# Kernel optimization log

Measured on AMD Instinct MI355X. Metric: run time of the kernel, lower is better.

## Reference

```python
import jax, jax.numpy as jnp
from jax import lax
import numpy as np

EPS_COS = 1e-8   # cosine-similarity eps (matches F.cosine_similarity default scale)
EPS_IN = 1e-5    # InstanceNorm2d default eps
NEG = -1e9


def _conv3(x, w, b):
    # x: [B,C,H,W], w: [O,I,3,3]
    y = lax.conv_general_dilated(x, w, (1, 1), 'SAME',
                                 dimension_numbers=('NCHW', 'OIHW', 'NCHW'))
    return y + b[None, :, None, None]


def _inorm(x):
    m = jnp.mean(x, axis=(2, 3), keepdims=True)
    v = jnp.var(x, axis=(2, 3), keepdims=True)
    return (x - m) * lax.rsqrt(v + EPS_IN)


def _shift(former, latter, mask):
    # former/latter: [B,C,H,W]; mask: [H,W] int (1 = hole).
    # For every masked pixel, find the most cosine-similar UNMASKED pixel in the
    # latter (known-region encoder) features and copy the former feature from it.
    B, C, H, W = former.shape
    L = H * W
    lat = lax.stop_gradient(latter).reshape(B, C, L)           # attention is non-differentiable
    latn = lat / (jnp.linalg.norm(lat, axis=1, keepdims=True) + EPS_COS)
    sim = jnp.einsum('bcm,bcn->bmn', latn, latn)               # [B,L,L] query m -> key n
    mflat = mask.reshape(L) > 0
    sim = jnp.where(mflat[None, None, :], NEG, sim)            # keys must be unmasked
    idx = jnp.argmax(sim, axis=-1)                             # [B,L]
    fflat = former.reshape(B, C, L)
    gathered = jnp.take_along_axis(fflat, jnp.broadcast_to(idx[:, None, :], (B, C, L)), axis=2)
    shift = jnp.where(mflat[None, None, :], gathered, 0.0)     # zeros outside the hole
    return shift.reshape(B, C, H, W)


def setup_inputs() -> dict:
    key = jax.random.key(0)
    ks = jax.random.split(key, 6)
    B, C, H, W = 8, 256, 64, 64
    inp = jax.random.normal(ks[0], (B, 2 * C, H, W), dtype=jnp.float32)
    mask = jax.random.randint(ks[1], (H, W), 0, 2, dtype=jnp.int32)
    s1 = 1.0 / float(np.sqrt(2 * C * 9))
    s2 = 1.0 / float(np.sqrt(C * 9))
    W1 = jax.random.uniform(ks[2], (C, 2 * C, 3, 3), jnp.float32, -s1, s1)
    b1 = jax.random.uniform(ks[3], (C,), jnp.float32, -s1, s1)
    W2 = jax.random.uniform(ks[4], (C, C, 3, 3), jnp.float32, -s2, s2)
    b2 = jax.random.uniform(ks[5], (C,), jnp.float32, -s2, s2)
    return {"input": inp, "mask": mask, "W1": W1, "b1": b1, "W2": W2, "b2": b2}


def reference(input, mask, W1, b1, W2, b2):
    C = input.shape[1] // 2
    F_c = input[:, :C]          # former (decoder) features
    F_s = input[:, C:]          # latter (encoder) features
    F_shift = _shift(F_c, F_s, mask)
    F_fuse = F_c * F_shift
    F_com = jnp.concatenate([F_c, F_fuse], axis=1)             # [B,2C,H,W]
    h = jax.nn.relu(_inorm(_conv3(F_com, W1, b1)))
    res = _inorm(_conv3(h, W2, b2))
    return jnp.concatenate([F_c + res, F_s], axis=1)
```

## Files before the change

### kernel.cpp

```cpp
#include <hip/hip_runtime.h>
#include <hip/hip_bf16.h>
#include <math.h>

#define L 4096
#define C 256
#define B 8

typedef __attribute__((ext_vector_type(8))) short bf16x8;
typedef __attribute__((ext_vector_type(8))) ushort u16x8;
typedef __attribute__((ext_vector_type(4))) float f32x4;

__device__ inline ushort f2bu(float f) { __hip_bfloat16 h = __float2bfloat16(f); return *(ushort*)&h; }
__device__ inline float bu2f(ushort u) { __hip_bfloat16 h; *(ushort*)&h = u; return __bfloat162float(h); }

__global__ __launch_bounds__(256) void compact_mask(
    const int* __restrict__ mask, int* __restrict__ counts,
    int* __restrict__ maskedOrig, int* __restrict__ unmaskOrig,
    int* __restrict__ posOf)
{
    __shared__ int smM[256], smU[256];
    int t = threadIdx.x;
    int flags[16];
    int cm = 0, cu = 0;
    for (int k = 0; k < 16; ++k) {
        int l = t * 16 + k;
        int f = mask[l] > 0;
        flags[k] = f;
        cm += f; cu += !f;
    }
    smM[t] = cm; smU[t] = cu;
    __syncthreads();
    for (int off = 1; off < 256; off <<= 1) {
        int vM = 0, vU = 0;
        if (t >= off) { vM = smM[t - off]; vU = smU[t - off]; }
        __syncthreads();
        smM[t] += vM; smU[t] += vU;
        __syncthreads();
    }
    if (t == 255) { counts[0] = smM[255]; counts[1] = smU[255]; }
    int pm = smM[t] - cm, pu = smU[t] - cu;
    for (int k = 0; k < 16; ++k) {
        int l = t * 16 + k;
        if (flags[k]) { maskedOrig[pm] = l; posOf[l] = pm; pm++; }
        else          { unmaskOrig[pu] = l; posOf[l] = pu; pu++; }
    }
}

__global__ __launch_bounds__(256) void norm_transpose(
    const float* __restrict__ input, const int* __restrict__ mask,
    const int* __restrict__ counts, const int* __restrict__ posOf,
    ushort* __restrict__ fsnh, ushort* __restrict__ fsnl)
{
    int bx = blockIdx.x;
    int b = bx >> 7;
    int l0 = (bx & 127) * 32;
    __shared__ float tile[256 * 33];
    __shared__ float part[8 * 33];
    __shared__ float denom[32];
    __shared__ int   rowdst[32];
    int t = threadIdx.x;
    int lsub = t & 31, cg = t >> 5;
    for (int cc = 0; cc < 256; cc += 8) {
        int c = cc + cg;
        tile[c * 33 + lsub] = input[((size_t)(b * 512 + 256 + c)) * L + l0 + lsub];
    }
    __syncthreads();
    float s = 0.f;
    for (int c = cg; c < 256; c += 8) { float v = tile[c * 33 + lsub]; s = fmaf(v, v, s); }
    part[cg * 33 + lsub] = s;
    __syncthreads();
    if (t < 32) {
        float s2 = 0.f;
        for (int g = 0; g < 8; ++g) s2 += part[g * 33 + t];
        denom[t] = sqrtf(s2) + 1e-8f;
        int l = l0 + t;
        int Nm = counts[0];
        rowdst[t] = (mask[l] > 0) ? posOf[l] : (Nm + posOf[l]);
    }
    __syncthreads();
    for (int ls = 0; ls < 32; ++ls) {
        int r = rowdst[ls];
        float d = denom[ls];
        float val = tile[t * 33 + ls] / d;
        ushort h = f2bu(val);
        float hf = bu2f(h);
        ushort lo = f2bu(val - hf);
        size_t o = ((size_t)b * L + r) * C + t;
        fsnh[o] = h;
        fsnl[o] = lo;
    }
}

__global__ __launch_bounds__(256, 2) void sim_argmax_v2(
    const ushort* __restrict__ hi, const ushort* __restrict__ lo,
    const int* __restrict__ counts,
    float* __restrict__ pval, int* __restrict__ pidx)
{
    __shared__ ushort ldsB[2 * 64 * 256];
    const int Nm = counts[0], Nu = counts[1];
    const int b = blockIdx.z;
    const int m0 = blockIdx.y * 64;
    const int half = blockIdx.x;
    const int t = threadIdx.x;
    const int w = t >> 6, l = t & 63;
    const int lm = l & 15, lk = l >> 4;
    const int key = (lm & 7) << 4;

    const int nct = (Nu + 63) >> 6;
    const int hs = (nct + 1) >> 1;
    const int cA = half * hs;
    const int cB = (half ? nct : hs);

    float bestv[4]; int bestn[4];
#pragma unroll
    for (int r = 0; r < 4; ++r) { bestv[r] = -3e38f; bestn[r] = 0; }

    if (m0 < Nm && cA < cB) {
        const char* bytesH = (const char*)hi;
        const char* bytesL = (const char*)lo;
        const size_t bL = (size_t)b * L;
        char* ldsc = (char*)ldsB;

#define STAGE(cc) do { \
    size_t gb = (bL + (size_t)Nm + (size_t)(cc) * 64) * 512; \
    _Pragma("unroll") \
    for (int i = 0; i < 8; ++i) { \
        int j = w * 8 + i; \
        int x = j * 1024 + l * 16; \
        int sx = x ^ (((x >> 9) & 7) << 4); \
        __builtin_amdgcn_global_load_lds((const __attribute__((address_space(1))) unsigned*)(bytesH + gb + sx), \
            (__attribute__((address_space(3))) unsigned*)(ldsc + j * 1024), 16, 0, 0); \
        __builtin_amdgcn_global_load_lds((const __attribute__((address_space(1))) unsigned*)(bytesL + gb + sx), \
            (__attribute__((address_space(3))) unsigned*)(ldsc + 32768 + j * 1024), 16, 0, 0); \
    } \
} while (0)

        STAGE(cA);

        const int rA = m0 + w * 16 + lm;
        bf16x8 ah[8], al[8];
        {
            const ushort* aH = hi + (bL + rA) * C + lk * 8;
            const ushort* aL = lo + (bL + rA) * C + lk * 8;
#pragma unroll
            for (int ks = 0; ks < 8; ++ks) {
                ah[ks] = *(const bf16x8*)(aH + ks * 32);
                al[ks] = *(const bf16x8*)(aL + ks * 32);
            }
        }

        for (int c = cA; c < cB; ++c) {
            asm volatile("s_waitcnt vmcnt(0)" ::: "memory");
            __syncthreads();
            f32x4 acc[4];
#pragma unroll
            for (int nf = 0; nf < 4; ++nf) acc[nf] = (f32x4){0.f, 0.f, 0.f, 0.f};
#pragma unroll
            for (int ks = 0; ks < 8; ++ks) {
                bf16x8 bh[4], bl[4];
#pragma unroll
                for (int nf = 0; nf < 4; ++nf) {
                    int row = nf * 16 + lm;
                    int addr = row * 512 + ((ks * 64 + lk * 16) ^ key);
                    bh[nf] = *(const bf16x8*)(ldsc + addr);
                    bl[nf] = *(const bf16x8*)(ldsc + 32768 + addr);
                }
#pragma unroll
                for (int nf = 0; nf < 4; ++nf)
                    acc[nf] = __builtin_amdgcn_mfma_f32_16x16x32_bf16(ah[ks], bh[nf], acc[nf], 0, 0, 0);
#pragma unroll
                for (int nf = 0; nf < 4; ++nf)
                    acc[nf] = __builtin_amdgcn_mfma_f32_16x16x32_bf16(ah[ks], bl[nf], acc[nf], 0, 0, 0);
#pragma unroll
                for (int nf = 0; nf < 4; ++nf)
                    acc[nf] = __builtin_amdgcn_mfma_f32_16x16x32_bf16(al[ks], bh[nf], acc[nf], 0, 0, 0);
            }
            __syncthreads();
            if (c + 1 < cB) STAGE(c + 1);
            int nbase = c * 64;
#pragma unroll
            for (int r = 0; r < 4; ++r) {
#pragma unroll
                for (int nf = 0; nf < 4; ++nf) {
                    int n = nbase + nf * 16 + lm;
                    float v = acc[nf][r];
                    if (n < Nu && v > bestv[r]) { bestv[r] = v; bestn[r] = n; }
                }
            }
        }
#undef STAGE
    }

    if (m0 >= Nm) return;
#pragma unroll
    for (int r = 0; r < 4; ++r) {
        float bv = bestv[r]; int bn = bestn[r];
#pragma unroll
        for (int mk = 1; mk < 16; mk <<= 1) {
            float ov = __shfl_xor(bv, mk, 64);
            int   on = __shfl_xor(bn, mk, 64);
            if (ov > bv || (ov == bv && on < bn)) { bv = ov; bn = on; }
        }
        if (lm == 0) {
            int m = m0 + w * 16 + lk * 4 + r;
            size_t o = ((size_t)(b * 4096 + m)) * 2 + half;
            pval[o] = bv; pidx[o] = bn;
        }
    }
}

__global__ __launch_bounds__(256) void argmax_reduce2(
    const float* __restrict__ pval, const int* __restrict__ pidx,
    const int* __restrict__ counts, const int* __restrict__ maskedOrig,
    const int* __restrict__ unmaskOrig, int* __restrict__ idxmap)
{
    int i = blockIdx.x * 256 + threadIdx.x;
    int b = i >> 12, m = i & 4095;
    int Nm = counts[0];
    if (m >= Nm) return;
    size_t base = (size_t)i * 2;
    float bv = pval[base]; int bn = pidx[base];
    float v1 = pval[base + 1];
    if (v1 > bv) { bv = v1; bn = pidx[base + 1]; }
    idxmap[(b << 12) + maskedOrig[m]] = unmaskOrig[bn];
}

__global__ __launch_bounds__(256) void wprep(
    const float* __restrict__ W1, const float* __restrict__ W2,
    ushort* __restrict__ W1bf, ushort* __restrict__ W2bf)
{
    int gid = blockIdx.x * 256 + threadIdx.x;
    const int N1 = 256 * 512 * 9;
    const int N2 = 256 * 256 * 9;
    if (gid < N1) {
        int ci = gid & 511; int rest = gid >> 9;
        int tau = rest % 9; int co = rest / 9;
        W1bf[gid] = f2bu(W1[((size_t)(co * 512 + ci)) * 9 + tau]);
    } else if (gid < N1 + N2) {
        int g = gid - N1;
        int ci = g & 255; int rest = g >> 8;
        int tau = rest % 9; int co = rest / 9;
        W2bf[g] = f2bu(W2[((size_t)(co * 256 + ci)) * 9 + tau]);
    }
}

__global__ __launch_bounds__(256) void in_prep1(
    const float* __restrict__ input, ushort* __restrict__ inT)
{
    int b = blockIdx.y;
    int p0 = blockIdx.x * 32;
    __shared__ float tile[256][33];
    int t = threadIdx.x;
    int pq = t & 7;
    for (int cc = 0; cc < 256; cc += 32) {
        int ci = cc + (t >> 3);
        float4 v = *(const float4*)(input + ((size_t)(b * 512 + ci)) * L + p0 + pq * 4);
        tile[ci][pq * 4 + 0] = v.x; tile[ci][pq * 4 + 1] = v.y;
        tile[ci][pq * 4 + 2] = v.z; tile[ci][pq * 4 + 3] = v.w;
    }
    __syncthreads();
    int c8 = t & 31;
    for (int pp = 0; pp < 32; pp += 8) {
        int pixloc = pp + (t >> 5);
        u16x8 u;
#pragma unroll
        for (int j = 0; j < 8; ++j) u[j] = f2bu(tile[c8 * 8 + j][pixloc]);
        *(u16x8*)(inT + ((size_t)(b * 4096 + p0 + pixloc)) * 512 + c8 * 8) = u;
    }
}

__global__ __launch_bounds__(256) void in_prep2(
    ushort* __restrict__ inT, const int* __restrict__ mask,
    const int* __restrict__ idxmap)
{
    int gid = blockIdx.x * 256 + threadIdx.x;
    int c8 = gid & 31;
    int pix = (gid >> 5) & 4095;
    int b = gid >> 17;
    u16x8 out8;
    if (mask[pix] > 0) {
        int n = idxmap[(b << 12) + pix];
        const ushort* rp = inT + ((size_t)(b * 4096 + pix)) * 512 + c8 * 8;
        const ushort* rn = inT + ((size_t)(b * 4096 + n)) * 512 + c8 * 8;
        u16x8 a = *(const u16x8*)rp;
        u16x8 bb = *(const u16x8*)rn;
#pragma unroll
        for (int j = 0; j < 8; ++j) out8[j] = f2bu(bu2f(a[j]) * bu2f(bb[j]));
    } else {
#pragma unroll
        for (int j = 0; j < 8; ++j) out8[j] = 0;
    }
    *(u16x8*)(inT + ((size_t)(b * 4096 + pix)) * 512 + 256 + c8 * 8) = out8;
}

template<int CKROW>
__global__ __launch_bounds__(256, 2) void conv_mfma(
    const ushort* __restrict__ Abf, const ushort* __restrict__ Wbf,
    float* __restrict__ outF, ushort* __restrict__ outH,
    float* __restrict__ psum, int store32)
{
    __shared__ float4 ldsv[62208 / 16];
    char* lds = (char*)ldsv;
    char* ldsB = lds + 25344;
    const int t = threadIdx.x;
    const int w = t >> 6;
    const int l = t & 63;
    const int lm = l & 15, lk = l >> 4;
    const int b = blockIdx.z;
    const int y0 = blockIdx.x * 4;
    const int c0 = blockIdx.y * 64;
    const int yw = y0 + w;
    const size_t abase = (size_t)b * 4096 * CKROW;

    f32x4 acc[4][4];
#pragma unroll
    for (int g = 0; g < 4; ++g)
#pragma unroll
        for (int nf = 0; nf < 4; ++nf) acc[g][nf] = (f32x4){0.f, 0.f, 0.f, 0.f};

    if (t < 48) {
        int r = t >> 3;
        int cX = ((t >> 2) & 1) ? 65 : 0;
        int k8 = t & 3;
        *(float4*)(lds + (r * 66 + cX) * 64 + ((k8 * 16) ^ ((cX & 3) << 4))) = (float4){0.f,0.f,0.f,0.f};
    }

    const int NKC = CKROW / 32;
    for (int kc = 0; kc < NKC; ++kc) {
        __syncthreads();
        {
            int x = t >> 2;
            int k8 = t & 3;
            int cX = x + 1;
            char* dbase = lds + cX * 64 + ((k8 * 16) ^ ((cX & 3) << 4));
#pragma unroll
            for (int r = 0; r < 6; ++r) {
                int yy = y0 - 1 + r;
                float4 v;
                if (yy >= 0 && yy < 64)
                    v = *(const float4*)(Abf + abase + (size_t)(yy * 64 + x) * CKROW + kc * 32 + k8 * 8);
                else
                    v = (float4){0.f, 0.f, 0.f, 0.f};
                *(float4*)(dbase + r * (66 * 64)) = v;
            }
        }
        {
            int cl = t >> 2;
            int k8 = t & 3;
            char* dbase = ldsB + cl * 64 + ((k8 * 16) ^ ((cl & 3) << 4));
            const ushort* sbase = Wbf + ((size_t)(c0 + cl) * 9) * CKROW + kc * 32 + k8 * 8;
#pragma unroll
            for (int tau = 0; tau < 9; ++tau) {
                *(float4*)(dbase + tau * (64 * 64)) = *(const float4*)(sbase + (size_t)tau * CKROW);
            }
        }
        __syncthreads();
#pragma unroll
        for (int ky = 0; ky < 3; ++ky) {
            int r = w + ky;
#pragma unroll
            for (int kx = 0; kx < 3; ++kx) {
                int tau = ky * 3 + kx;
                bf16x8 bfr[4];
#pragma unroll
                for (int nf = 0; nf < 4; ++nf) {
                    int cl = nf * 16 + lm;
                    bfr[nf] = *(bf16x8*)(ldsB + (tau * 64 + cl) * 64 + ((lk * 16) ^ ((cl & 3) << 4)));
                }
#pragma unroll
                for (int g = 0; g < 4; ++g) {
                    int cX = g * 16 + lm + kx;
                    bf16x8 afr = *(bf16x8*)(lds + (r * 66 + cX) * 64 + ((lk * 16) ^ ((cX & 3) << 4)));
#pragma unroll
                    for (int nf = 0; nf < 4; ++nf)
                        acc[g][nf] = __builtin_amdgcn_mfma_f32_16x16x32_bf16(afr, bfr[nf], acc[g][nf], 0, 0, 0);
                }
            }
        }
    }

    if (store32) {
#pragma unroll
        for (int g = 0; g < 4; ++g)
#pragma unroll
            for (int nf = 0; nf < 4; ++nf) {
                int cout = c0 + nf * 16 + lm;
#pragma unroll
                for (int r = 0; r < 4; ++r) {
                    int pix = yw * 64 + g * 16 + lk * 4 + r;
                    outF[((size_t)(b * 4096 + pix)) * 256 + cout] = acc[g][nf][r];
                }
            }
    } else {
#pragma unroll
        for (int g = 0; g < 4; ++g)
#pragma unroll
            for (int nf = 0; nf < 4; ++nf) {
                int cout = c0 + nf * 16 + lm;
#pragma unroll
                for (int r = 0; r < 4; ++r) {
                    int pix = yw * 64 + g * 16 + lk * 4 + r;
                    outH[((size_t)(b * 4096 + pix)) * 256 + cout] = f2bu(acc[g][nf][r]);
                }
            }
    }

    float s[4], q[4];
#pragma unroll
    for (int nf = 0; nf < 4; ++nf) {
        float ss = 0.f, qq = 0.f;
#pragma unroll
        for (int g = 0; g < 4; ++g)
#pragma unroll
            for (int r = 0; r < 4; ++r) { float v = acc[g][nf][r]; ss += v; qq = fmaf(v, v, qq); }
        ss += __shfl_xor(ss, 16, 64); ss += __shfl_xor(ss, 32, 64);
        qq += __shfl_xor(qq, 16, 64); qq += __shfl_xor(qq, 32, 64);
        s[nf] = ss; q[nf] = qq;
    }
    __syncthreads();
    float* S = (float*)lds;
    float* Q = (float*)(lds + 1024);
    if (l < 16) {
#pragma unroll
        for (int nf = 0; nf < 4; ++nf) {
            S[w * 64 + nf * 16 + l] = s[nf];
            Q[w * 64 + nf * 16 + l] = q[nf];
        }
    }
    __syncthreads();
    if (t < 64) {
        float ts = 0.f, tq = 0.f;
#pragma unroll
        for (int w2 = 0; w2 < 4; ++w2) { ts += S[w2 * 64 + t]; tq += Q[w2 * 64 + t]; }
        size_t o = (((size_t)(b * 256 + c0 + t)) * 16 + blockIdx.x) * 2;
        psum[o] = ts; psum[o + 1] = tq;
    }
}

__global__ __launch_bounds__(256) void stats_reduce(
    const float* __restrict__ psum, float* __restrict__ mrs)
{
    int b = blockIdx.x;
    int c = threadIdx.x;
    float s = 0.f, q = 0.f;
    size_t base = ((size_t)(b * 256 + c)) * 16;
    for (int k = 0; k < 16; ++k) { s += psum[(base + k) * 2]; q += psum[(base + k) * 2 + 1]; }
    float mean = s * (1.f / 4096.f);
    float var = q * (1.f / 4096.f) - mean * mean;
    float rs = rsqrtf(var + 1e-5f);
    mrs[(b * 256 + c) * 2] = mean;
    mrs[(b * 256 + c) * 2 + 1] = rs;
}

__global__ __launch_bounds__(256) void norm1_apply(
    const float* __restrict__ h_raw, const float* __restrict__ mrs,
    ushort* __restrict__ hbf)
{
    int gid = blockIdx.x * 256 + threadIdx.x;
    int c4 = gid & 63;
    int pix = (gid >> 6) & 4095;
    int b = gid >> 18;
    float4 hv = *(const float4*)(h_raw + (((size_t)(b * 4096 + pix)) << 8) + c4 * 4);
    const float4* mv = (const float4*)(mrs + (size_t)b * 512);
    float4 m0 = mv[c4 * 2];
    float4 m1 = mv[c4 * 2 + 1];
    float z0 = (hv.x - m0.x) * m0.y;
    float z1 = (hv.y - m0.z) * m0.w;
    float z2 = (hv.z - m1.x) * m1.y;
    float z3 = (hv.w - m1.z) * m1.w;
    ushort4 o;
    o.x = f2bu(z0 > 0.f ? z0 : 0.f);
    o.y = f2bu(z1 > 0.f ? z1 : 0.f);
    o.z = f2bu(z2 > 0.f ? z2 : 0.f);
    o.w = f2bu(z3 > 0.f ? z3 : 0.f);
    *(ushort4*)(hbf + (((size_t)(b * 4096 + pix)) << 8) + c4 * 4) = o;
}

__global__ __launch_bounds__(256) void finalize(
    const ushort* __restrict__ resbf, const float* __restrict__ mrs,
    const float* __restrict__ input, float* __restrict__ out)
{
    int b = blockIdx.y;
    int p0 = blockIdx.x * 32;
    __shared__ float tileT[256][33];
    int t = threadIdx.x;
    int c8 = t & 31;
    for (int pp = 0; pp < 32; pp += 8) {
        int pixloc = pp + (t >> 5);
        u16x8 u = *(const u16x8*)(resbf + (((size_t)(b * 4096 + p0 + pixloc)) << 8) + c8 * 8);
#pragma unroll
        for (int j = 0; j < 8; ++j) tileT[c8 * 8 + j][pixloc] = bu2f(u[j]);
    }
    __syncthreads();
    int pq = t & 7;
    for (int cc = 0; cc < 256; cc += 32) {
        int c = cc + (t >> 3);
        float m = mrs[(b * 256 + c) * 2];
        float rs = mrs[(b * 256 + c) * 2 + 1];
        size_t off = ((size_t)(b * 512 + c)) * L + p0 + pq * 4;
        float4 f = *(const float4*)(input + off);
        float4 o;
        o.x = f.x + (tileT[c][pq * 4 + 0] - m) * rs;
        o.y = f.y + (tileT[c][pq * 4 + 1] - m) * rs;
        o.z = f.z + (tileT[c][pq * 4 + 2] - m) * rs;
        o.w = f.w + (tileT[c][pq * 4 + 3] - m) * rs;
        *(float4*)(out + off) = o;
    }
}

__global__ __launch_bounds__(256) void copy_fs(
    const float* __restrict__ input, float* __restrict__ out)
{
    size_t i = (size_t)blockIdx.x * 256 + threadIdx.x;
    size_t b = i >> 18;
    size_t r = i & 262143;
    size_t o = ((size_t)(b * 512 + 256)) * 1024 + r;
    const float4* s = (const float4*)input;
    float4* d = (float4*)out;
    d[o] = s[o];
}

extern "C" void kernel_launch(void* const* d_in, const int* in_sizes, int n_in,
                              void* d_out, int out_size, void* d_ws, size_t ws_size,
                              hipStream_t stream) {
    const float* input = (const float*)d_in[0];
    const int*   mask  = (const int*)d_in[1];
    const float* W1    = (const float*)d_in[2];
    const float* W2    = (const float*)d_in[4];
    float* out = (float*)d_out;
    (void)in_sizes; (void)n_in; (void)out_size; (void)ws_size;

    char* ob = (char*)d_out;
    char* wp = (char*)d_ws;

    ushort* fsnh = (ushort*)ob;
    ushort* fsnl = (ushort*)(ob + 16777216);
    float*  pval = (float*)(ob + 33554432);
    int*    pidx = (int*)(ob + 37748736);
    ushort* inT  = (ushort*)ob;
    float*  h_raw = (float*)(ob + 33554432);
    ushort* hbf  = (ushort*)ob;

    ushort* resbf  = (ushort*)wp;
    ushort* W1bf   = (ushort*)(wp + 16777216);
    ushort* W2bf   = (ushort*)(wp + 19136512);
    float*  psum1  = (float*)(wp + 20316160);
    float*  psum2  = (float*)(wp + 20578304);
    float*  mrs1   = (float*)(wp + 20840448);
    float*  mrs2   = (float*)(wp + 20856832);
    int* counts     = (int*)(wp + 20873216);
    int* maskedOrig = counts + 4;
    int* unmaskOrig = maskedOrig + L;
    int* posOf      = unmaskOrig + L;
    int* idxmap     = posOf + L;

    compact_mask<<<1, 256, 0, stream>>>(mask, counts, maskedOrig, unmaskOrig, posOf);
    norm_transpose<<<1024, 256, 0, stream>>>(input, mask, counts, posOf, fsnh, fsnl);
    sim_argmax_v2<<<dim3(2, 64, 8), 256, 0, stream>>>(fsnh, fsnl, counts, pval, pidx);
    argmax_reduce2<<<128, 256, 0, stream>>>(pval, pidx, counts, maskedOrig, unmaskOrig, idxmap);
    wprep<<<6912, 256, 0, stream>>>(W1, W2, W1bf, W2bf);
    in_prep1<<<dim3(128, 8), 256, 0, stream>>>(input, inT);
    in_prep2<<<4096, 256, 0, stream>>>(inT, mask, idxmap);
    conv_mfma<512><<<dim3(16, 4, 8), 256, 0, stream>>>(inT, W1bf, h_raw, (ushort*)nullptr, psum1, 1);
    stats_reduce<<<8, 256, 0, stream>>>(psum1, mrs1);
    norm1_apply<<<8192, 256, 0, stream>>>(h_raw, mrs1, hbf);
    conv_mfma<256><<<dim3(16, 4, 8), 256, 0, stream>>>(hbf, W2bf, (float*)nullptr, resbf, psum2, 0);
    stats_reduce<<<8, 256, 0, stream>>>(psum2, mrs2);
    finalize<<<dim3(128, 8), 256, 0, stream>>>(resbf, mrs2, input, out);
    copy_fs<<<8192, 256, 0, stream>>>(input, out);
}
```

Baseline: 282.1 us.

## Double-buffer sim-argmax LDS tiles with 512-thread blocks; store conv1 output as bf16

```diff
diff --git a/kernel.cpp b/kernel.cpp
--- a/kernel.cpp
+++ b/kernel.cpp
@@ -91,12 +91,12 @@
     }
 }
 
-__global__ __launch_bounds__(256, 2) void sim_argmax_v2(
+__global__ __launch_bounds__(512, 1) void sim_argmax_v3(
     const ushort* __restrict__ hi, const ushort* __restrict__ lo,
     const int* __restrict__ counts,
     float* __restrict__ pval, int* __restrict__ pidx)
 {
-    __shared__ ushort ldsB[2 * 64 * 256];
+    __shared__ ushort ldsB[65536];
     const int Nm = counts[0], Nu = counts[1];
     const int b = blockIdx.z;
     const int m0 = blockIdx.y * 64;
@@ -104,97 +104,99 @@
     const int t = threadIdx.x;
     const int w = t >> 6, l = t & 63;
     const int lm = l & 15, lk = l >> 4;
-    const int key = (lm & 7) << 4;
+    const int mh = w & 1, nq = w >> 1;
 
     const int nct = (Nu + 63) >> 6;
     const int hs = (nct + 1) >> 1;
-    const int cA = half * hs;
-    const int cB = (half ? nct : hs);
-
-    float bestv[4]; int bestn[4];
-#pragma unroll
-    for (int r = 0; r < 4; ++r) { bestv[r] = -3e38f; bestn[r] = 0; }
-
-    if (m0 < Nm && cA < cB) {
+    const int cA = half * hs, cB = half ? nct : hs;
+
+    float bestv0[4], bestv1[4]; int bestn0[4], bestn1[4];
+#pragma unroll
+    for (int r = 0; r < 4; ++r) {
+        bestv0[r] = -3e38f; bestn0[r] = 0;
+        bestv1[r] = -3e38f; bestn1[r] = 0;
+    }
+
+    if (m0 >= Nm) return;
+
+    if (cA < cB) {
+        char* ldsc = (char*)ldsB;
         const char* bytesH = (const char*)hi;
         const char* bytesL = (const char*)lo;
         const size_t bL = (size_t)b * L;
-        char* ldsc = (char*)ldsB;
-
-#define STAGE(cc) do { \
+
+#define STAGE(bufofs, cc) do { \
     size_t gb = (bL + (size_t)Nm + (size_t)(cc) * 64) * 512; \
     _Pragma("unroll") \
-    for (int i = 0; i < 8; ++i) { \
-        int j = w * 8 + i; \
-        int x = j * 1024 + l * 16; \
-        int sx = x ^ (((x >> 9) & 7) << 4); \
+    for (int i = 0; i < 4; ++i) { \
+        int xu = w * 4096 + i * 1024; \
+        int xl = xu + l * 16; \
+        int sx = xl ^ (((xl >> 9) & 7) << 4); \
         __builtin_amdgcn_global_load_lds((const __attribute__((address_space(1))) unsigned*)(bytesH + gb + sx), \
-            (__attribute__((address_space(3))) unsigned*)(ldsc + j * 1024), 16, 0, 0); \
+            (__attribute__((address_space(3))) unsigned*)(ldsc + (bufofs) + xu), 16, 0, 0); \
         __builtin_amdgcn_global_load_lds((const __attribute__((address_space(1))) unsigned*)(bytesL + gb + sx), \
-            (__attribute__((address_space(3))) unsigned*)(ldsc + 32768 + j * 1024), 16, 0, 0); \
+            (__attribute__((address_space(3))) unsigned*)(ldsc + (bufofs) + 32768 + xu), 16, 0, 0); \
     } \
 } while (0)
 
-        STAGE(cA);
-
-        const int rA = m0 + w * 16 + lm;
-        bf16x8 ah[8], al[8];
+        STAGE(0, cA);
+
+        const int rA0 = m0 + mh * 32 + lm;
+        bf16x8 ah0[8], al0[8], ah1[8], al1[8];
         {
-            const ushort* aH = hi + (bL + rA) * C + lk * 8;
-            const ushort* aL = lo + (bL + rA) * C + lk * 8;
+            const ushort* aH0 = hi + (bL + rA0) * C + lk * 8;
+            const ushort* aL0 = lo + (bL + rA0) * C + lk * 8;
+            const ushort* aH1 = aH0 + 16 * C;
+            const ushort* aL1 = aL0 + 16 * C;
 #pragma unroll
             for (int ks = 0; ks < 8; ++ks) {
-                ah[ks] = *(const bf16x8*)(aH + ks * 32);
-                al[ks] = *(const bf16x8*)(aL + ks * 32);
-            }
-        }
+                ah0[ks] = *(const bf16x8*)(aH0 + ks * 32);
+                al0[ks] = *(const bf16x8*)(aL0 + ks * 32);
+                ah1[ks] = *(const bf16x8*)(aH1 + ks * 32);
+                al1[ks] = *(const bf16x8*)(aL1 + ks * 32);
+            }
+        }
+
+        const int row = nq * 16 + lm;
+        const int key = (row & 7) << 4;
 
         for (int c = cA; c < cB; ++c) {
+            int bo = ((c - cA) & 1) * 65536;
             asm volatile("s_waitcnt vmcnt(0)" ::: "memory");
             __syncthreads();
-            f32x4 acc[4];
-#pragma unroll
-            for (int nf = 0; nf < 4; ++nf) acc[nf] = (f32x4){0.f, 0.f, 0.f, 0.f};
+            if (c + 1 < cB) STAGE(bo ^ 65536, c + 1);
+            const char* bhp = ldsc + bo + row * 512;
+            const char* blp = bhp + 32768;
+            f32x4 acc0 = (f32x4){0.f, 0.f, 0.f, 0.f};
+            f32x4 acc1 = (f32x4){0.f, 0.f, 0.f, 0.f};
 #pragma unroll
             for (int ks = 0; ks < 8; ++ks) {
-                bf16x8 bh[4], bl[4];
-#pragma unroll
-                for (int nf = 0; nf < 4; ++nf) {
-                    int row = nf * 16 + lm;
-                    int addr = row * 512 + ((ks * 64 + lk * 16) ^ key);
-                    bh[nf] = *(const bf16x8*)(ldsc + addr);
-                    bl[nf] = *(const bf16x8*)(ldsc + 32768 + addr);
-                }
-#pragma unroll
-                for (int nf = 0; nf < 4; ++nf)
-                    acc[nf] = __builtin_amdgcn_mfma_f32_16x16x32_bf16(ah[ks], bh[nf], acc[nf], 0, 0, 0);
-#pragma unroll
-                for (int nf = 0; nf < 4; ++nf)
-                    acc[nf] = __builtin_amdgcn_mfma_f32_16x16x32_bf16(ah[ks], bl[nf], acc[nf], 0, 0, 0);
-#pragma unroll
-                for (int nf = 0; nf < 4; ++nf)
-                    acc[nf] = __builtin_amdgcn_mfma_f32_16x16x32_bf16(al[ks], bh[nf], acc[nf], 0, 0, 0);
-            }
-            __syncthreads();
-            if (c + 1 < cB) STAGE(c + 1);
-            int nbase = c * 64;
+                int off = (ks * 64 + lk * 16) ^ key;
+                bf16x8 bh = *(const bf16x8*)(bhp + off);
+                bf16x8 bl = *(const bf16x8*)(blp + off);
+                acc0 = __builtin_amdgcn_mfma_f32_16x16x32_bf16(ah0[ks], bh, acc0, 0, 0, 0);
+                acc0 = __builtin_amdgcn_mfma_f32_16x16x32_bf16(ah0[ks], bl, acc0, 0, 0, 0);
+                acc0 = __builtin_amdgcn_mfma_f32_16x16x32_bf16(al0[ks], bh, acc0, 0, 0, 0);
+                acc1 = __builtin_amdgcn_mfma_f32_16x16x32_bf16(ah1[ks], bh, acc1, 0, 0, 0);
+                acc1 = __builtin_amdgcn_mfma_f32_16x16x32_bf16(ah1[ks], bl, acc1, 0, 0, 0);
+                acc1 = __builtin_amdgcn_mfma_f32_16x16x32_bf16(al1[ks], bh, acc1, 0, 0, 0);
+            }
+            int n = c * 64 + nq * 16 + lm;
+            bool nv = n < Nu;
 #pragma unroll
             for (int r = 0; r < 4; ++r) {
-#pragma unroll
-                for (int nf = 0; nf < 4; ++nf) {
-                    int n = nbase + nf * 16 + lm;
-                    float v = acc[nf][r];
-                    if (n < Nu && v > bestv[r]) { bestv[r] = v; bestn[r] = n; }
-                }
+                float v0 = acc0[r];
+                if (nv && v0 > bestv0[r]) { bestv0[r] = v0; bestn0[r] = n; }
+                float v1 = acc1[r];
+                if (nv && v1 > bestv1[r]) { bestv1[r] = v1; bestn1[r] = n; }
             }
         }
 #undef STAGE
     }
 
-    if (m0 >= Nm) return;
 #pragma unroll
     for (int r = 0; r < 4; ++r) {
-        float bv = bestv[r]; int bn = bestn[r];
+        float bv = bestv0[r]; int bn = bestn0[r];
 #pragma unroll
         for (int mk = 1; mk < 16; mk <<= 1) {
             float ov = __shfl_xor(bv, mk, 64);
@@ -202,26 +204,40 @@
             if (ov > bv || (ov == bv && on < bn)) { bv = ov; bn = on; }
         }
         if (lm == 0) {
-            int m = m0 + w * 16 + lk * 4 + r;
-            size_t o = ((size_t)(b * 4096 + m)) * 2 + half;
+            int m = m0 + mh * 32 + lk * 4 + r;
+            size_t o = ((size_t)(b * 4096 + m)) * 8 + half * 4 + nq;
             pval[o] = bv; pidx[o] = bn;
         }
-    }
-}
-
-__global__ __launch_bounds__(256) void argmax_reduce2(
+        bv = bestv1[r]; bn = bestn1[r];
+#pragma unroll
+        for (int mk = 1; mk < 16; mk <<= 1) {
+            float ov = __shfl_xor(bv, mk, 64);
+            int   on = __shfl_xor(bn, mk, 64);
+            if (ov > bv || (ov == bv && on < bn)) { bv = ov; bn = on; }
+        }
+        if (lm == 0) {
+            int m = m0 + mh * 32 + 16 + lk * 4 + r;
+            size_t o = ((size_t)(b * 4096 + m)) * 8 + half * 4 + nq;
+            pval[o] = bv; pidx[o] = bn;
+        }
+    }
+}
+
+__global__ __launch_bounds__(256) void argmax_reduce8(
     const float* __restrict__ pval, const int* __restrict__ pidx,
     const int* __restrict__ counts, const int* __restrict__ maskedOrig,
     const int* __restrict__ unmaskOrig, int* __restrict__ idxmap)
 {
     int i = blockIdx.x * 256 + threadIdx.x;
     int b = i >> 12, m = i & 4095;
-    int Nm = counts[0];
-    if (m >= Nm) return;
-    size_t base = (size_t)i * 2;
+    if (m >= counts[0]) return;
+    size_t base = (size_t)i * 8;
     float bv = pval[base]; int bn = pidx[base];
-    float v1 = pval[base + 1];
-    if (v1 > bv) { bv = v1; bn = pidx[base + 1]; }
+#pragma unroll
+    for (int p = 1; p < 8; ++p) {
+        float v = pval[base + p]; int n2 = pidx[base + p];
+        if (v > bv || (v == bv && n2 < bn)) { bv = v; bn = n2; }
+    }
     idxmap[(b << 12) + maskedOrig[m]] = unmaskOrig[bn];
 }
 
@@ -453,27 +469,23 @@
 }
 
 __global__ __launch_bounds__(256) void norm1_apply(
-    const float* __restrict__ h_raw, const float* __restrict__ mrs,
+    const ushort* __restrict__ hraw, const float* __restrict__ mrs,
     ushort* __restrict__ hbf)
 {
     int gid = blockIdx.x * 256 + threadIdx.x;
-    int c4 = gid & 63;
-    int pix = (gid >> 6) & 4095;
-    int b = gid >> 18;
-    float4 hv = *(const float4*)(h_raw + (((size_t)(b * 4096 + pix)) << 8) + c4 * 4);
-    const float4* mv = (const float4*)(mrs + (size_t)b * 512);
-    float4 m0 = mv[c4 * 2];
-    float4 m1 = mv[c4 * 2 + 1];
-    float z0 = (hv.x - m0.x) * m0.y;
-    float z1 = (hv.y - m0.z) * m0.w;
-    float z2 = (hv.z - m1.x) * m1.y;
-    float z3 = (hv.w - m1.z) * m1.w;
-    ushort4 o;
-    o.x = f2bu(z0 > 0.f ? z0 : 0.f);
-    o.y = f2bu(z1 > 0.f ? z1 : 0.f);
-    o.z = f2bu(z2 > 0.f ? z2 : 0.f);
-    o.w = f2bu(z3 > 0.f ? z3 : 0.f);
-    *(ushort4*)(hbf + (((size_t)(b * 4096 + pix)) << 8) + c4 * 4) = o;
+    int c8 = gid & 31;
+    int pix = (gid >> 5) & 4095;
+    int b = gid >> 17;
+    size_t off = (((size_t)(b * 4096 + pix)) << 8) + c8 * 8;
+    u16x8 v = *(const u16x8*)(hraw + off);
+    const float* mb = mrs + (size_t)b * 512 + c8 * 16;
+    u16x8 o;
+#pragma unroll
+    for (int j = 0; j < 8; ++j) {
+        float z = (bu2f(v[j]) - mb[j * 2]) * mb[j * 2 + 1];
+        o[j] = f2bu(z > 0.f ? z : 0.f);
+    }
+    *(u16x8*)(hbf + off) = o;
 }
 
 __global__ __launch_bounds__(256) void finalize(
@@ -538,7 +550,7 @@
     float*  pval = (float*)(ob + 33554432);
     int*    pidx = (int*)(ob + 37748736);
     ushort* inT  = (ushort*)ob;
-    float*  h_raw = (float*)(ob + 33554432);
+    ushort* hraw = (ushort*)(ob + 33554432);
     ushort* hbf  = (ushort*)ob;
 
     ushort* resbf  = (ushort*)wp;
@@ -556,14 +568,14 @@
 
     compact_mask<<<1, 256, 0, stream>>>(mask, counts, maskedOrig, unmaskOrig, posOf);
     norm_transpose<<<1024, 256, 0, stream>>>(input, mask, counts, posOf, fsnh, fsnl);
-    sim_argmax_v2<<<dim3(2, 64, 8), 256, 0, stream>>>(fsnh, fsnl, counts, pval, pidx);
-    argmax_reduce2<<<128, 256, 0, stream>>>(pval, pidx, counts, maskedOrig, unmaskOrig, idxmap);
+    sim_argmax_v3<<<dim3(2, 64, 8), 512, 0, stream>>>(fsnh, fsnl, counts, pval, pidx);
+    argmax_reduce8<<<128, 256, 0, stream>>>(pval, pidx, counts, maskedOrig, unmaskOrig, idxmap);
     wprep<<<6912, 256, 0, stream>>>(W1, W2, W1bf, W2bf);
     in_prep1<<<dim3(128, 8), 256, 0, stream>>>(input, inT);
     in_prep2<<<4096, 256, 0, stream>>>(inT, mask, idxmap);
-    conv_mfma<512><<<dim3(16, 4, 8), 256, 0, stream>>>(inT, W1bf, h_raw, (ushort*)nullptr, psum1, 1);
+    conv_mfma<512><<<dim3(16, 4, 8), 256, 0, stream>>>(inT, W1bf, (float*)nullptr, hraw, psum1, 0);
     stats_reduce<<<8, 256, 0, stream>>>(psum1, mrs1);
-    norm1_apply<<<8192, 256, 0, stream>>>(h_raw, mrs1, hbf);
+    norm1_apply<<<4096, 256, 0, stream>>>(hraw, mrs1, hbf);
     conv_mfma<256><<<dim3(16, 4, 8), 256, 0, stream>>>(hbf, W2bf, (float*)nullptr, resbf, psum2, 0);
     stats_reduce<<<8, 256, 0, stream>>>(psum2, mrs2);
     finalize<<<dim3(128, 8), 256, 0, stream>>>(resbf, mrs2, input, out);
```

Result: slower. 293.8 us (+4.1%).

## Store conv1 output as bf16, widen LDS swizzle, vectorize norm1 apply

Applied to the files above, without the earlier changes.

```diff
diff --git a/kernel.cpp b/kernel.cpp
--- a/kernel.cpp
+++ b/kernel.cpp
@@ -91,7 +91,7 @@
     }
 }
 
-__global__ __launch_bounds__(256, 2) void sim_argmax_v2(
+__global__ __launch_bounds__(256, 2) void sim_argmax_v6(
     const ushort* __restrict__ hi, const ushort* __restrict__ lo,
     const int* __restrict__ counts,
     float* __restrict__ pval, int* __restrict__ pidx)
@@ -104,12 +104,11 @@
     const int t = threadIdx.x;
     const int w = t >> 6, l = t & 63;
     const int lm = l & 15, lk = l >> 4;
-    const int key = (lm & 7) << 4;
+    const int key = lm << 4;
 
     const int nct = (Nu + 63) >> 6;
     const int hs = (nct + 1) >> 1;
-    const int cA = half * hs;
-    const int cB = (half ? nct : hs);
+    const int cA = half * hs, cB = half ? nct : hs;
 
     float bestv[4]; int bestn[4];
 #pragma unroll
@@ -127,7 +126,7 @@
     for (int i = 0; i < 8; ++i) { \
         int j = w * 8 + i; \
         int x = j * 1024 + l * 16; \
-        int sx = x ^ (((x >> 9) & 7) << 4); \
+        int sx = x ^ (((x >> 9) & 15) << 4); \
         __builtin_amdgcn_global_load_lds((const __attribute__((address_space(1))) unsigned*)(bytesH + gb + sx), \
             (__attribute__((address_space(3))) unsigned*)(ldsc + j * 1024), 16, 0, 0); \
         __builtin_amdgcn_global_load_lds((const __attribute__((address_space(1))) unsigned*)(bytesL + gb + sx), \
@@ -216,12 +215,11 @@
 {
     int i = blockIdx.x * 256 + threadIdx.x;
     int b = i >> 12, m = i & 4095;
-    int Nm = counts[0];
-    if (m >= Nm) return;
+    if (m >= counts[0]) return;
     size_t base = (size_t)i * 2;
     float bv = pval[base]; int bn = pidx[base];
-    float v1 = pval[base + 1];
-    if (v1 > bv) { bv = v1; bn = pidx[base + 1]; }
+    float v1 = pval[base + 1]; int n1 = pidx[base + 1];
+    if (v1 > bv || (v1 == bv && n1 < bn)) { bv = v1; bn = n1; }
     idxmap[(b << 12) + maskedOrig[m]] = unmaskOrig[bn];
 }
 
@@ -453,27 +451,23 @@
 }
 
 __global__ __launch_bounds__(256) void norm1_apply(
-    const float* __restrict__ h_raw, const float* __restrict__ mrs,
+    const ushort* __restrict__ hraw, const float* __restrict__ mrs,
     ushort* __restrict__ hbf)
 {
     int gid = blockIdx.x * 256 + threadIdx.x;
-    int c4 = gid & 63;
-    int pix = (gid >> 6) & 4095;
-    int b = gid >> 18;
-    float4 hv = *(const float4*)(h_raw + (((size_t)(b * 4096 + pix)) << 8) + c4 * 4);
-    const float4* mv = (const float4*)(mrs + (size_t)b * 512);
-    float4 m0 = mv[c4 * 2];
-    float4 m1 = mv[c4 * 2 + 1];
-    float z0 = (hv.x - m0.x) * m0.y;
-    float z1 = (hv.y - m0.z) * m0.w;
-    float z2 = (hv.z - m1.x) * m1.y;
-    float z3 = (hv.w - m1.z) * m1.w;
-    ushort4 o;
-    o.x = f2bu(z0 > 0.f ? z0 : 0.f);
-    o.y = f2bu(z1 > 0.f ? z1 : 0.f);
-    o.z = f2bu(z2 > 0.f ? z2 : 0.f);
-    o.w = f2bu(z3 > 0.f ? z3 : 0.f);
-    *(ushort4*)(hbf + (((size_t)(b * 4096 + pix)) << 8) + c4 * 4) = o;
+    int c8 = gid & 31;
+    int pix = (gid >> 5) & 4095;
+    int b = gid >> 17;
+    size_t off = (((size_t)(b * 4096 + pix)) << 8) + c8 * 8;
+    u16x8 v = *(const u16x8*)(hraw + off);
+    const float* mb = mrs + (size_t)b * 512 + c8 * 16;
+    u16x8 o;
+#pragma unroll
+    for (int j = 0; j < 8; ++j) {
+        float z = (bu2f(v[j]) - mb[j * 2]) * mb[j * 2 + 1];
+        o[j] = f2bu(z > 0.f ? z : 0.f);
+    }
+    *(u16x8*)(hbf + off) = o;
 }
 
 __global__ __launch_bounds__(256) void finalize(
@@ -538,7 +532,7 @@
     float*  pval = (float*)(ob + 33554432);
     int*    pidx = (int*)(ob + 37748736);
     ushort* inT  = (ushort*)ob;
-    float*  h_raw = (float*)(ob + 33554432);
+    ushort* hraw = (ushort*)(ob + 33554432);
     ushort* hbf  = (ushort*)ob;
 
     ushort* resbf  = (ushort*)wp;
@@ -556,14 +550,14 @@
 
     compact_mask<<<1, 256, 0, stream>>>(mask, counts, maskedOrig, unmaskOrig, posOf);
     norm_transpose<<<1024, 256, 0, stream>>>(input, mask, counts, posOf, fsnh, fsnl);
-    sim_argmax_v2<<<dim3(2, 64, 8), 256, 0, stream>>>(fsnh, fsnl, counts, pval, pidx);
+    sim_argmax_v6<<<dim3(2, 64, 8), 256, 0, stream>>>(fsnh, fsnl, counts, pval, pidx);
     argmax_reduce2<<<128, 256, 0, stream>>>(pval, pidx, counts, maskedOrig, unmaskOrig, idxmap);
     wprep<<<6912, 256, 0, stream>>>(W1, W2, W1bf, W2bf);
     in_prep1<<<dim3(128, 8), 256, 0, stream>>>(input, inT);
     in_prep2<<<4096, 256, 0, stream>>>(inT, mask, idxmap);
-    conv_mfma<512><<<dim3(16, 4, 8), 256, 0, stream>>>(inT, W1bf, h_raw, (ushort*)nullptr, psum1, 1);
+    conv_mfma<512><<<dim3(16, 4, 8), 256, 0, stream>>>(inT, W1bf, (float*)nullptr, hraw, psum1, 0);
     stats_reduce<<<8, 256, 0, stream>>>(psum1, mrs1);
-    norm1_apply<<<8192, 256, 0, stream>>>(h_raw, mrs1, hbf);
+    norm1_apply<<<4096, 256, 0, stream>>>(hraw, mrs1, hbf);
     conv_mfma<256><<<dim3(16, 4, 8), 256, 0, stream>>>(hbf, W2bf, (float*)nullptr, resbf, psum2, 0);
     stats_reduce<<<8, 256, 0, stream>>>(psum2, mrs2);
     finalize<<<dim3(128, 8), 256, 0, stream>>>(resbf, mrs2, input, out);
```

Measured after the change: 272.8 us. 1.03x faster.
